# Performance work log

Hardware: AMD Instinct MI355X
Metric: run time of the kernel (lower is better)

## Reference

```python
import jax, jax.numpy as jnp
import numpy as np

B, T, C, H = 8, 2048, 1024, 64  # batch, block_size(=seq), embedding_dim, head_size

def setup_inputs() -> dict:
    key = jax.random.key(0)
    kx, kk, kq, kv = jax.random.split(key, 4)
    s = 1.0 / np.sqrt(C)
    return {
        "x": jax.random.normal(kx, (B, T, C), dtype=jnp.float32),
        "Wk": jax.random.normal(kk, (C, H), dtype=jnp.float32) * s,
        "Wq": jax.random.normal(kq, (C, H), dtype=jnp.float32) * s,
        "Wv": jax.random.normal(kv, (C, H), dtype=jnp.float32) * s,
    }

def reference(x, Wk, Wq, Wv):
    # projections: [B,T,C] @ [C,H] -> [B,T,H]
    k = jnp.einsum("btc,ch->bth", x, Wk)
    q = jnp.einsum("btc,ch->bth", x, Wq)
    v = jnp.einsum("btc,ch->bth", x, Wv)
    # scores: [B,T,T], scaled by head_size^-0.5
    wei = jnp.einsum("bth,bsh->bts", q, k) * (k.shape[-1] ** -0.5)
    # causal mask (lower-triangular keep)
    causal = jnp.tril(jnp.ones((T, T), dtype=bool))
    wei = jnp.where(causal[None, :, :], wei, -jnp.inf)
    wei = jax.nn.softmax(wei, axis=-1)
    # dropout_rate=0.0 -> identity
    out = jnp.einsum("bts,bsh->bth", wei, v)
    return out
```

## Files before the change

### kernel.cpp

```cpp
#include <hip/hip_runtime.h>

#define NB 8
#define NT 2048
#define NC 1024
#define NH 64
#define BT (NB*NT)

typedef __bf16 bf16x8 __attribute__((ext_vector_type(8)));
typedef float  f32x4  __attribute__((ext_vector_type(4)));
typedef unsigned short us8 __attribute__((ext_vector_type(8)));

__device__ __forceinline__ unsigned short f2bf(float f) {
  unsigned u = __builtin_bit_cast(unsigned, f);
  u = (u + 0x7FFFu + ((u >> 16) & 1u)) >> 16;
  return (unsigned short)u;
}

__device__ __forceinline__ bf16x8 ld_frag(const unsigned short* p) {
  return __builtin_bit_cast(bf16x8, *(const us8*)p);
}

__global__ __launch_bounds__(256) void wconv_kernel(
    const float* __restrict__ Wk, const float* __restrict__ Wq,
    const float* __restrict__ Wv, unsigned short* __restrict__ Wt)
{
  __shared__ unsigned short T[64][72];
  const int t = threadIdx.x;
  const int mat = blockIdx.x >> 4;
  const int k0 = (blockIdx.x & 15) * 64;
  const float* __restrict__ W = (mat == 0) ? Wq : (mat == 1) ? Wk : Wv;
  const int kk = t >> 2, h0 = (t & 3) * 16;
  const float* src = &W[(size_t)(k0 + kk) * NH + h0];
#pragma unroll
  for (int j = 0; j < 4; ++j) {
    const float4 v = *(const float4*)(src + j*4);
    T[h0 + j*4 + 0][kk] = f2bf(v.x);
    T[h0 + j*4 + 1][kk] = f2bf(v.y);
    T[h0 + j*4 + 2][kk] = f2bf(v.z);
    T[h0 + j*4 + 3][kk] = f2bf(v.w);
  }
  __syncthreads();
  const int h = t >> 2, c0 = (t & 3) * 16;
  unsigned short* dst = &Wt[(size_t)(mat*64 + h) * NC + k0 + c0];
  *(us8*)dst       = *(const us8*)&T[h][c0];
  *(us8*)(dst + 8) = *(const us8*)&T[h][c0 + 8];
}

__global__ __launch_bounds__(256) void proj_kernel(
    const float* __restrict__ x, const unsigned short* __restrict__ Wt,
    unsigned short* __restrict__ qkv)
{
  __shared__ float Asmf[2][32][68];
  __shared__ unsigned short Bsm[2][192][72];
  __shared__ unsigned short Vb[64][40];

  const int t = threadIdx.x, w = t >> 6, lane = t & 63;
  const int m0 = blockIdx.x * 32;
  const int fr = lane & 15, fo = (lane >> 4) * 8, rg = (lane >> 4) * 4;

  f32x4 acc[2][3];
#pragma unroll
  for (int m = 0; m < 2; ++m)
#pragma unroll
    for (int n = 0; n < 3; ++n) acc[m][n] = (f32x4){0.f, 0.f, 0.f, 0.f};

  const int srow0 = t >> 4, scol = (t & 15) * 4;
  const int srow1 = srow0 + 16;
  const int br = t >> 3, bkc = (t & 7) * 8;

  {
    const float4 a = *(const float4*)&x[(size_t)(m0 + srow0) * NC + scol];
    const float4 b = *(const float4*)&x[(size_t)(m0 + srow1) * NC + scol];
    *(f32x4*)&Asmf[0][srow0][scol] = (f32x4){a.x, a.y, a.z, a.w};
    *(f32x4*)&Asmf[0][srow1][scol] = (f32x4){b.x, b.y, b.z, b.w};
#pragma unroll
    for (int i = 0; i < 6; ++i) {
      const int c = t + 256*i, r = (c >> 3) + (i >= 3 ? 96 : 0) - (i >= 3 ? 96 : 0);
      (void)r;
      const int rr = c >> 3, kc = (c & 7) * 8;
      *(us8*)&Bsm[0][rr][kc] = *(const us8*)&Wt[(size_t)rr * NC + kc];
    }
  }
  __syncthreads();

  for (int s = 0; s < 16; ++s) {
    const int cur = s & 1;
    if (s < 15) {
      const int k1 = (s + 1) * 64;
      const float4 a = *(const float4*)&x[(size_t)(m0 + srow0) * NC + k1 + scol];
      const float4 b = *(const float4*)&x[(size_t)(m0 + srow1) * NC + k1 + scol];
      *(f32x4*)&Asmf[cur^1][srow0][scol] = (f32x4){a.x, a.y, a.z, a.w};
      *(f32x4*)&Asmf[cur^1][srow1][scol] = (f32x4){b.x, b.y, b.z, b.w};
#pragma unroll
      for (int i = 0; i < 6; ++i) {
        const int c = t + 256*i, rr = c >> 3, kc = (c & 7) * 8;
        *(us8*)&Bsm[cur^1][rr][kc] = *(const us8*)&Wt[(size_t)rr * NC + k1 + kc];
      }
    }

    bf16x8 af[2][2], bfr[2][3];
#pragma unroll
    for (int m = 0; m < 2; ++m)
#pragma unroll
      for (int ks = 0; ks < 2; ++ks) {
        const f32x4 lo = *(const f32x4*)&Asmf[cur][m*16 + fr][ks*32 + fo];
        const f32x4 hi = *(const f32x4*)&Asmf[cur][m*16 + fr][ks*32 + fo + 4];
        bf16x8 v;
        v[0] = (__bf16)lo[0]; v[1] = (__bf16)lo[1]; v[2] = (__bf16)lo[2]; v[3] = (__bf16)lo[3];
        v[4] = (__bf16)hi[0]; v[5] = (__bf16)hi[1]; v[6] = (__bf16)hi[2]; v[7] = (__bf16)hi[3];
        af[m][ks] = v;
      }
#pragma unroll
    for (int ks = 0; ks < 2; ++ks)
#pragma unroll
      for (int n = 0; n < 3; ++n)
        bfr[ks][n] = ld_frag(&Bsm[cur][w*48 + n*16 + fr][ks*32 + fo]);
#pragma unroll
    for (int ks = 0; ks < 2; ++ks)
#pragma unroll
      for (int m = 0; m < 2; ++m)
#pragma unroll
        for (int n = 0; n < 3; ++n)
          acc[m][n] = __builtin_amdgcn_mfma_f32_16x16x32_bf16(af[m][ks], bfr[ks][n], acc[m][n], 0, 0, 0);
    __syncthreads();
  }

#pragma unroll
  for (int m = 0; m < 2; ++m)
#pragma unroll
    for (int n = 0; n < 3; ++n) {
      const int col = w*48 + n*16;
      if (col < 128) {
        unsigned short* op = qkv + (size_t)(col >> 6) * BT * NH;
        const int h = (col & 63) + fr;
#pragma unroll
        for (int r = 0; r < 4; ++r)
          op[(size_t)(m0 + m*16 + rg + r) * NH + h] = f2bf(acc[m][n][r]);
      } else {
#pragma unroll
        for (int r = 0; r < 4; ++r)
          Vb[(col - 128) + fr][m*16 + rg + r] = f2bf(acc[m][n][r]);
      }
    }
  __syncthreads();
  {
    unsigned short* vt = qkv + (size_t)2 * BT * NH;
    const int h = t >> 2, c = (t & 3) * 8;
    *(us8*)&vt[(size_t)h * BT + m0 + c] = *(const us8*)&Vb[h][c];
  }
}

__global__ __launch_bounds__(512) void attn_kernel(
    const unsigned short* __restrict__ qkv, float* __restrict__ out)
{
  __shared__ unsigned short Psm[8][16][72];
  __shared__ float co[8][16][68];
  __shared__ float cl[8][16];

  const int t = threadIdx.x, w = t >> 6, lane = t & 63;
  const int b = blockIdx.y;
  const int j0 = blockIdx.x;
  const unsigned short* __restrict__ qp = qkv;
  const unsigned short* __restrict__ kp = qkv + (size_t)BT * NH;
  const unsigned short* __restrict__ vt = qkv + (size_t)2 * BT * NH;
  const int fr = lane & 15, fo = (lane >> 4) * 8, rg = (lane >> 4) * 4;

#pragma unroll 1
  for (int ph = 0; ph < 2; ++ph) {
    const int j = ph ? (127 - j0) : j0;
    const int q0 = j * 16;
    const int ntiles = (j >> 2) + 1;

    bf16x8 aq0, aq1;
    {
      const size_t qoff = ((size_t)b * NT + q0 + fr) * NH;
      aq0 = ld_frag(&qp[qoff + fo]);
      aq1 = ld_frag(&qp[qoff + 32 + fo]);
    }

    f32x4 o[4];
#pragma unroll
    for (int n = 0; n < 4; ++n) o[n] = (f32x4){0.f, 0.f, 0.f, 0.f};
    float lp[4] = {0.f, 0.f, 0.f, 0.f};

    for (int kt = w; kt < ntiles; kt += 8) {
      const int kv0 = kt * 64;

      f32x4 s[4];
#pragma unroll
      for (int n = 0; n < 4; ++n) s[n] = (f32x4){0.f, 0.f, 0.f, 0.f};
#pragma unroll
      for (int n = 0; n < 4; ++n) {
        const size_t koff = ((size_t)b*NT + kv0 + n*16 + fr) * NH + fo;
        s[n] = __builtin_amdgcn_mfma_f32_16x16x32_bf16(aq0, ld_frag(&kp[koff]), s[n], 0, 0, 0);
        s[n] = __builtin_amdgcn_mfma_f32_16x16x32_bf16(aq1, ld_frag(&kp[koff + 32]), s[n], 0, 0, 0);
      }

#pragma unroll
      for (int n = 0; n < 4; ++n)
#pragma unroll
        for (int r = 0; r < 4; ++r) s[n][r] = __expf(s[n][r] * 0.125f);

      if (kt == ntiles - 1) {
#pragma unroll
        for (int n = 0; n < 4; ++n) {
          const int col = kv0 + n*16 + fr;
#pragma unroll
          for (int r = 0; r < 4; ++r)
            if (col > q0 + rg + r) s[n][r] = 0.f;
        }
      }

#pragma unroll
      for (int r = 0; r < 4; ++r)
        lp[r] += (s[0][r] + s[1][r]) + (s[2][r] + s[3][r]);

#pragma unroll
      for (int n = 0; n < 4; ++n)
#pragma unroll
        for (int r = 0; r < 4; ++r)
          Psm[w][rg + r][n*16 + fr] = f2bf(s[n][r]);

      bf16x8 pa0 = ld_frag(&Psm[w][fr][fo]);
      bf16x8 pa1 = ld_frag(&Psm[w][fr][32 + fo]);

#pragma unroll
      for (int n = 0; n < 4; ++n) {
        const size_t voff = (size_t)(n*16 + fr) * BT + (size_t)b*NT + kv0 + fo;
        o[n] = __builtin_amdgcn_mfma_f32_16x16x32_bf16(pa0, ld_frag(&vt[voff]), o[n], 0, 0, 0);
        o[n] = __builtin_amdgcn_mfma_f32_16x16x32_bf16(pa1, ld_frag(&vt[voff + 32]), o[n], 0, 0, 0);
      }
    }

#pragma unroll
    for (int r = 0; r < 4; ++r) {
#pragma unroll
      for (int off = 1; off < 16; off <<= 1) lp[r] += __shfl_xor(lp[r], off);
    }
    if (fr == 0) {
#pragma unroll
      for (int r = 0; r < 4; ++r) cl[w][rg + r] = lp[r];
    }
#pragma unroll
    for (int n = 0; n < 4; ++n)
#pragma unroll
      for (int r = 0; r < 4; ++r) co[w][rg + r][n*16 + fr] = o[n][r];
    __syncthreads();

    {
      const int row = (t >> 4) & 15, c0 = (t & 15) * 4;
      if (t < 256) {
        float l = 0.f;
#pragma unroll
        for (int ww = 0; ww < 8; ++ww) l += cl[ww][row];
        const float inv = 1.f / l;
        float4 ov = {0.f, 0.f, 0.f, 0.f};
#pragma unroll
        for (int ww = 0; ww < 8; ++ww) {
          ov.x += co[ww][row][c0+0]; ov.y += co[ww][row][c0+1];
          ov.z += co[ww][row][c0+2]; ov.w += co[ww][row][c0+3];
        }
        ov.x *= inv; ov.y *= inv; ov.z *= inv; ov.w *= inv;
        *(float4*)&out[((size_t)b*NT + q0 + row) * NH + c0] = ov;
      }
    }
    if (ph == 0) __syncthreads();
  }
}

extern "C" void kernel_launch(void* const* d_in, const int* in_sizes, int n_in,
                              void* d_out, int out_size, void* d_ws, size_t ws_size,
                              hipStream_t stream) {
  (void)in_sizes; (void)n_in; (void)out_size; (void)ws_size;
  const float* x  = (const float*)d_in[0];
  const float* Wk = (const float*)d_in[1];
  const float* Wq = (const float*)d_in[2];
  const float* Wv = (const float*)d_in[3];
  unsigned short* qkv = (unsigned short*)d_ws;
  unsigned short* Wt  = qkv + (size_t)3 * BT * NH;

  wconv_kernel<<<48, 256, 0, stream>>>(Wk, Wq, Wv, Wt);
  proj_kernel<<<BT/32, 256, 0, stream>>>(x, Wt, qkv);
  attn_kernel<<<dim3(64, NB), 512, 0, stream>>>(qkv, (float*)d_out);
}
```

Measured before the change: 147.6 us.

## Restructure attention into 32-row query blocks with register-prefetched K/V staged in LDS

The attention kernel now handles 32 query rows per block. The 8 waves are split into 2 query groups times 4 key-tile partitions, and key tiles shrink to 32. Each wave prefetches its next K/V tile into registers while it computes on the current one, which it stages through per-wave shared memory so the MFMA fragments are loaded from LDS instead of global memory. The grid is halved and the final reduction now merges 4 partial results per row instead of 8. The trade-offs are more LDS traffic and shared-memory footprint, and fewer blocks in flight.

```diff
diff --git a/kernel.cpp b/kernel.cpp
--- a/kernel.cpp
+++ b/kernel.cpp
@@ -66,7 +66,6 @@
 
   const int srow0 = t >> 4, scol = (t & 15) * 4;
   const int srow1 = srow0 + 16;
-  const int br = t >> 3, bkc = (t & 7) * 8;
 
   {
     const float4 a = *(const float4*)&x[(size_t)(m0 + srow0) * NC + scol];
@@ -75,9 +74,7 @@
     *(f32x4*)&Asmf[0][srow1][scol] = (f32x4){b.x, b.y, b.z, b.w};
 #pragma unroll
     for (int i = 0; i < 6; ++i) {
-      const int c = t + 256*i, r = (c >> 3) + (i >= 3 ? 96 : 0) - (i >= 3 ? 96 : 0);
-      (void)r;
-      const int rr = c >> 3, kc = (c & 7) * 8;
+      const int c = t + 256*i, rr = c >> 3, kc = (c & 7) * 8;
       *(us8*)&Bsm[0][rr][kc] = *(const us8*)&Wt[(size_t)rr * NC + kc];
     }
   }
@@ -153,23 +150,28 @@
 __global__ __launch_bounds__(512) void attn_kernel(
     const unsigned short* __restrict__ qkv, float* __restrict__ out)
 {
-  __shared__ unsigned short Psm[8][16][72];
+  __shared__ unsigned short Ksm[8][32][72];
+  __shared__ unsigned short Vsm[8][64][36];
+  __shared__ unsigned short Psm[8][16][36];
   __shared__ float co[8][16][68];
   __shared__ float cl[8][16];
 
   const int t = threadIdx.x, w = t >> 6, lane = t & 63;
   const int b = blockIdx.y;
   const int j0 = blockIdx.x;
+  const int g = w & 1, p = w >> 1;
   const unsigned short* __restrict__ qp = qkv;
   const unsigned short* __restrict__ kp = qkv + (size_t)BT * NH;
   const unsigned short* __restrict__ vt = qkv + (size_t)2 * BT * NH;
   const int fr = lane & 15, fo = (lane >> 4) * 8, rg = (lane >> 4) * 4;
+  const int krow = lane >> 3, kcol = (lane & 7) * 8;
+  const int vrow = lane >> 2, vcol = (lane & 3) * 8;
 
 #pragma unroll 1
   for (int ph = 0; ph < 2; ++ph) {
-    const int j = ph ? (127 - j0) : j0;
-    const int q0 = j * 16;
-    const int ntiles = (j >> 2) + 1;
+    const int j = ph ? (63 - j0) : j0;
+    const int ntiles = j + 1;
+    const int q0 = j*32 + g*16;
 
     bf16x8 aq0, aq1;
     {
@@ -183,27 +185,57 @@
     for (int n = 0; n < 4; ++n) o[n] = (f32x4){0.f, 0.f, 0.f, 0.f};
     float lp[4] = {0.f, 0.f, 0.f, 0.f};
 
-    for (int kt = w; kt < ntiles; kt += 8) {
-      const int kv0 = kt * 64;
-
-      f32x4 s[4];
-#pragma unroll
-      for (int n = 0; n < 4; ++n) s[n] = (f32x4){0.f, 0.f, 0.f, 0.f};
-#pragma unroll
-      for (int n = 0; n < 4; ++n) {
-        const size_t koff = ((size_t)b*NT + kv0 + n*16 + fr) * NH + fo;
-        s[n] = __builtin_amdgcn_mfma_f32_16x16x32_bf16(aq0, ld_frag(&kp[koff]), s[n], 0, 0, 0);
-        s[n] = __builtin_amdgcn_mfma_f32_16x16x32_bf16(aq1, ld_frag(&kp[koff + 32]), s[n], 0, 0, 0);
-      }
-
-#pragma unroll
-      for (int n = 0; n < 4; ++n)
+    us8 kreg[4], vreg[4];
+    {
+      const int kt0 = (p < ntiles) ? p : (ntiles - 1);
+      const size_t kb = (size_t)b * NT + kt0 * 32;
+#pragma unroll
+      for (int i = 0; i < 4; ++i)
+        kreg[i] = *(const us8*)&kp[(kb + i*8 + krow) * NH + kcol];
+#pragma unroll
+      for (int i = 0; i < 4; ++i)
+        vreg[i] = *(const us8*)&vt[(size_t)(i*16 + vrow) * BT + kb + vcol];
+    }
+
+    for (int kt = p; kt < ntiles; kt += 4) {
+      const int kv0 = kt * 32;
+#pragma unroll
+      for (int i = 0; i < 4; ++i)
+        *(us8*)&Ksm[w][i*8 + krow][kcol] = kreg[i];
+#pragma unroll
+      for (int i = 0; i < 4; ++i)
+        *(us8*)&Vsm[w][i*16 + vrow][vcol] = vreg[i];
+
+      {
+        const int nk = (kt + 4 < ntiles) ? kt + 4 : kt;
+        const size_t kb = (size_t)b * NT + nk * 32;
+#pragma unroll
+        for (int i = 0; i < 4; ++i)
+          kreg[i] = *(const us8*)&kp[(kb + i*8 + krow) * NH + kcol];
+#pragma unroll
+        for (int i = 0; i < 4; ++i)
+          vreg[i] = *(const us8*)&vt[(size_t)(i*16 + vrow) * BT + kb + vcol];
+      }
+
+      f32x4 s[2];
+#pragma unroll
+      for (int n = 0; n < 2; ++n) s[n] = (f32x4){0.f, 0.f, 0.f, 0.f};
+#pragma unroll
+      for (int n = 0; n < 2; ++n) {
+        bf16x8 k0 = ld_frag(&Ksm[w][n*16 + fr][fo]);
+        bf16x8 k1 = ld_frag(&Ksm[w][n*16 + fr][32 + fo]);
+        s[n] = __builtin_amdgcn_mfma_f32_16x16x32_bf16(aq0, k0, s[n], 0, 0, 0);
+        s[n] = __builtin_amdgcn_mfma_f32_16x16x32_bf16(aq1, k1, s[n], 0, 0, 0);
+      }
+
+#pragma unroll
+      for (int n = 0; n < 2; ++n)
 #pragma unroll
         for (int r = 0; r < 4; ++r) s[n][r] = __expf(s[n][r] * 0.125f);
 
       if (kt == ntiles - 1) {
 #pragma unroll
-        for (int n = 0; n < 4; ++n) {
+        for (int n = 0; n < 2; ++n) {
           const int col = kv0 + n*16 + fr;
 #pragma unroll
           for (int r = 0; r < 4; ++r)
@@ -212,23 +244,19 @@
       }
 
 #pragma unroll
-      for (int r = 0; r < 4; ++r)
-        lp[r] += (s[0][r] + s[1][r]) + (s[2][r] + s[3][r]);
-
-#pragma unroll
-      for (int n = 0; n < 4; ++n)
+      for (int r = 0; r < 4; ++r) lp[r] += s[0][r] + s[1][r];
+
+#pragma unroll
+      for (int n = 0; n < 2; ++n)
 #pragma unroll
         for (int r = 0; r < 4; ++r)
           Psm[w][rg + r][n*16 + fr] = f2bf(s[n][r]);
 
-      bf16x8 pa0 = ld_frag(&Psm[w][fr][fo]);
-      bf16x8 pa1 = ld_frag(&Psm[w][fr][32 + fo]);
-
+      bf16x8 pa = ld_frag(&Psm[w][fr][fo]);
 #pragma unroll
       for (int n = 0; n < 4; ++n) {
-        const size_t voff = (size_t)(n*16 + fr) * BT + (size_t)b*NT + kv0 + fo;
-        o[n] = __builtin_amdgcn_mfma_f32_16x16x32_bf16(pa0, ld_frag(&vt[voff]), o[n], 0, 0, 0);
-        o[n] = __builtin_amdgcn_mfma_f32_16x16x32_bf16(pa1, ld_frag(&vt[voff + 32]), o[n], 0, 0, 0);
+        bf16x8 bv = ld_frag(&Vsm[w][n*16 + fr][fo]);
+        o[n] = __builtin_amdgcn_mfma_f32_16x16x32_bf16(pa, bv, o[n], 0, 0, 0);
       }
     }
 
@@ -248,21 +276,16 @@
     __syncthreads();
 
     {
-      const int row = (t >> 4) & 15, c0 = (t & 15) * 4;
-      if (t < 256) {
-        float l = 0.f;
-#pragma unroll
-        for (int ww = 0; ww < 8; ++ww) l += cl[ww][row];
-        const float inv = 1.f / l;
-        float4 ov = {0.f, 0.f, 0.f, 0.f};
-#pragma unroll
-        for (int ww = 0; ww < 8; ++ww) {
-          ov.x += co[ww][row][c0+0]; ov.y += co[ww][row][c0+1];
-          ov.z += co[ww][row][c0+2]; ov.w += co[ww][row][c0+3];
-        }
-        ov.x *= inv; ov.y *= inv; ov.z *= inv; ov.w *= inv;
-        *(float4*)&out[((size_t)b*NT + q0 + row) * NH + c0] = ov;
-      }
+      const int row = t >> 4, c0 = (t & 15) * 4;
+      const int g2 = row >> 4, rr = row & 15;
+      const float l = (cl[g2][rr] + cl[2 + g2][rr]) + (cl[4 + g2][rr] + cl[6 + g2][rr]);
+      const float inv = 1.f / l;
+      float4 ov;
+      ov.x = ((co[g2][rr][c0+0] + co[2+g2][rr][c0+0]) + (co[4+g2][rr][c0+0] + co[6+g2][rr][c0+0])) * inv;
+      ov.y = ((co[g2][rr][c0+1] + co[2+g2][rr][c0+1]) + (co[4+g2][rr][c0+1] + co[6+g2][rr][c0+1])) * inv;
+      ov.z = ((co[g2][rr][c0+2] + co[2+g2][rr][c0+2]) + (co[4+g2][rr][c0+2] + co[6+g2][rr][c0+2])) * inv;
+      ov.w = ((co[g2][rr][c0+3] + co[2+g2][rr][c0+3]) + (co[4+g2][rr][c0+3] + co[6+g2][rr][c0+3])) * inv;
+      *(float4*)&out[((size_t)b*NT + j*32 + row) * NH + c0] = ov;
     }
     if (ph == 0) __syncthreads();
   }
@@ -281,5 +304,5 @@
 
   wconv_kernel<<<48, 256, 0, stream>>>(Wk, Wq, Wv, Wt);
   proj_kernel<<<BT/32, 256, 0, stream>>>(x, Wt, qkv);
-  attn_kernel<<<dim3(64, NB), 512, 0, stream>>>(qkv, (float*)d_out);
-}
+  attn_kernel<<<dim3(32, NB), 512, 0, stream>>>(qkv, (float*)d_out);
+}
```

Measured after the change: 147.7 us. No clear change (+0.0%).
